# Optimization experiments

Measured on AMD Instinct MI355X. Metric: run time of the kernel, lower is better.

Reference implementation:

```python
import jax, jax.numpy as jnp
import numpy as np

B, N, DH, DG, HID, K_STEPS, CURV = 256, 2048, 128, 256, 256, 2, 1.0
SC = CURV ** 0.5
SCALE = 1.0 / (DH ** 0.5)
LN_EPS = 1e-5


def _artanh(x):
    return jnp.arctanh(jnp.clip(x, -1.0 + 1e-5, 1.0 - 1e-5))


def logmap0(x, sc=SC):
    n = jnp.maximum(jnp.linalg.norm(x, axis=-1, keepdims=True), 1e-7)
    return x * (_artanh(sc * n) / (sc * n))


def expmap0(v, sc=SC):
    n = jnp.maximum(jnp.linalg.norm(v, axis=-1, keepdims=True), 1e-7)
    return v * (jnp.tanh(sc * n) / (sc * n))


def setup_inputs() -> dict:
    key = jax.random.key(0)
    ks = jax.random.split(key, 16)

    def lin(k, out_d, in_d):
        return (jax.random.normal(k, (out_d, in_d), jnp.float32) * (in_d ** -0.5))

    demo_hyp = expmap0(0.1 * jax.random.normal(ks[0], (B, N, DH), jnp.float32))
    rho_g = jax.random.normal(ks[1], (B, DG), jnp.float32)
    return {
        "demo_hyp": demo_hyp,
        "rho_g": rho_g,
        "seed_g_w": lin(ks[2], DH, DG),
        "seed_g_b": jnp.zeros((DH,), jnp.float32),
        "seed_d_w": lin(ks[3], DH, DH),
        "pool_wq_w": lin(ks[4], DH, DH),
        "pool_wk_w": lin(ks[5], DH, DH),
        "pool_wv_w": lin(ks[6], DH, DH),
        "q_u_w": lin(ks[7], DH, DH),
        "q_g_w": lin(ks[8], DH, DG),
        "q_g_b": jnp.zeros((DH,), jnp.float32),
        "kv_w": lin(ks[9], DH, DH),
        "mlp_w1": lin(ks[10], HID, DH),
        "mlp_b1": jnp.zeros((HID,), jnp.float32),
        "mlp_w2": lin(ks[11], DH, HID),
        "mlp_b2": jnp.zeros((DH,), jnp.float32),
        "ln_g": jnp.ones((DH,), jnp.float32),
        "ln_b": jnp.zeros((DH,), jnp.float32),
    }


def reference(demo_hyp, rho_g, seed_g_w, seed_g_b, seed_d_w,
              pool_wq_w, pool_wk_w, pool_wv_w, q_u_w, q_g_w, q_g_b,
              kv_w, mlp_w1, mlp_b1, mlp_w2, mlp_b2, ln_g, ln_b):
    demo_tan = logmap0(demo_hyp)                       # (B,N,Dh)

    # seed: attention-pool demos with rho_g query
    q_seed = rho_g @ seed_g_w.T + seed_g_b             # (B,Dh)
    qk = q_seed @ pool_wq_w.T                          # (B,Dh)
    Kp = demo_tan @ pool_wk_w.T                        # (B,N,Dh)
    a = jax.nn.softmax(jnp.einsum('bd,bnd->bn', qk, Kp) * SCALE, axis=-1)
    Vp = demo_tan @ pool_wv_w.T
    pooled = jnp.einsum('bn,bnd->bd', a, Vp)           # (B,Dh)
    u = expmap0(q_seed + pooled @ seed_d_w.T)

    for _ in range(K_STEPS):
        u_tan = logmap0(u)
        mu = jnp.mean(u_tan, axis=-1, keepdims=True)
        var = jnp.var(u_tan, axis=-1, keepdims=True)
        u_tan = (u_tan - mu) * jax.lax.rsqrt(var + LN_EPS) * ln_g + ln_b
        q = u_tan @ q_u_w.T + rho_g @ q_g_w.T + q_g_b
        Kmat = demo_tan @ kv_w.T                       # keys == values
        att = jax.nn.softmax(jnp.einsum('bd,bnd->bn', q, Kmat) * SCALE, axis=-1)
        delta = jnp.einsum('bn,bnd->bd', att, Kmat)
        upd = jax.nn.gelu(delta @ mlp_w1.T + mlp_b1, approximate=False) @ mlp_w2.T + mlp_b2
        u = expmap0(u_tan + upd)
    return u
```

## Files before the change

kernel.cpp:

```cpp
#include <hip/hip_runtime.h>
#include <cstddef>
#include <cstdint>

#define B 256
#define N 2048
#define DH 128
#define DG 256
#define HID 256
#define WAVES 8
#define TPB (WAVES * 64)
#define RPI (WAVES * 8)
#define KIT (N / RPI)
#define SCALE 0.08838834764831845f
#define LN_EPS 1e-5f
#define TAN_NORM_MAX 6.2f


__device__ __forceinline__ float artanh_clip(float a) {
  a = fminf(a, 1.0f - 1e-5f);
  return 0.5f * __logf((1.0f + a) / (1.0f - a));
}

__device__ __forceinline__ float logmap_scale(float n2) {
  float nc = fmaxf(sqrtf(n2), 1e-7f);
  return artanh_clip(nc) / nc;
}

__device__ __forceinline__ float row16_sum(float x) {
  x += __int_as_float(__builtin_amdgcn_update_dpp(0, __float_as_int(x), 0x128, 0xF, 0xF, true));
  x += __int_as_float(__builtin_amdgcn_update_dpp(0, __float_as_int(x), 0x124, 0xF, 0xF, true));
  x += __int_as_float(__builtin_amdgcn_update_dpp(0, __float_as_int(x), 0x122, 0xF, 0xF, true));
  x += __int_as_float(__builtin_amdgcn_update_dpp(0, __float_as_int(x), 0x121, 0xF, 0xF, true));
  return x;
}

__device__ __forceinline__ float wave_allsum(float v) {
#pragma unroll
  for (int m = 1; m < 64; m <<= 1) v += __shfl_xor(v, m);
  return v;
}

__device__ __forceinline__ float dot128(const float* __restrict__ wrow,
                                        const float* __restrict__ x) {
  const float4* a = (const float4*)wrow;
  const float4* v = (const float4*)x;
  float s = 0.f;
#pragma unroll
  for (int j = 0; j < 32; ++j) {
    float4 u = a[j], b = v[j];
    s += u.x * b.x + u.y * b.y + u.z * b.z + u.w * b.w;
  }
  return s;
}

__device__ __forceinline__ float dot256(const float* __restrict__ wrow,
                                        const float* __restrict__ x) {
  const float4* a = (const float4*)wrow;
  const float4* v = (const float4*)x;
  float s = 0.f;
#pragma unroll
  for (int j = 0; j < 64; ++j) {
    float4 u = a[j], b = v[j];
    s += u.x * b.x + u.y * b.y + u.z * b.z + u.w * b.w;
  }
  return s;
}


__global__ __launch_bounds__(TPB, 2) void fused_refiner(
    const float* __restrict__ demo, const float* __restrict__ rho,
    const float* __restrict__ seed_g_w, const float* __restrict__ seed_g_b,
    const float* __restrict__ seed_d_w, const float* __restrict__ pool_wq_w,
    const float* __restrict__ pool_wk_w, const float* __restrict__ pool_wv_w,
    const float* __restrict__ q_u_w, const float* __restrict__ q_g_w,
    const float* __restrict__ q_g_b, const float* __restrict__ kv_w,
    const float* __restrict__ mlp_w1, const float* __restrict__ mlp_b1,
    const float* __restrict__ mlp_w2, const float* __restrict__ mlp_b2,
    const float* __restrict__ ln_g, const float* __restrict__ ln_b,
    float* __restrict__ out) {
  const int b = blockIdx.x;
  const int tid = threadIdx.x;
  const int w = tid >> 6;
  const int lane = tid & 63;
  const int g = lane >> 4;
  const int il = lane & 15;

  __shared__ __align__(16) float s_rho[DG];
  __shared__ __align__(16) float s_x[DH];
  __shared__ __align__(16) float s_y[DH];
  __shared__ __align__(16) float s_h[HID];
  __shared__ __align__(16) float s_ut[DH];
  __shared__ __align__(16) float s_qseed[DH];
  __shared__ __align__(16) float s_qvec[DH];
  __shared__ __align__(16) float s_fold[WAVES][DH];
  __shared__ float s_l[WAVES];
  __shared__ float s_red[WAVES];
  __shared__ float s_Mb;

  auto bsumAll = [&](float v) -> float {
    v = wave_allsum(v);
    if (lane == 0) s_red[w] = v;
    __syncthreads();
    float r = s_red[0] + s_red[1] + s_red[2] + s_red[3] +
              s_red[4] + s_red[5] + s_red[6] + s_red[7];
    __syncthreads();
    return r;
  };

  auto ln_query = [&](float v) {
    float n2 = bsumAll(tid < DH ? v * v : 0.f);
    float u = 0.f, ut = 0.f;
    if (tid < DH) {
      float nc = fmaxf(sqrtf(n2), 1e-7f);
      u = v * (tanhf(nc) / nc);
    }
    float nu2 = bsumAll(tid < DH ? u * u : 0.f);
    if (tid < DH) {
      float nuc = fmaxf(sqrtf(nu2), 1e-7f);
      ut = u * (artanh_clip(nuc) / nuc);
    }
    float mu = bsumAll(tid < DH ? ut : 0.f) * (1.0f / DH);
    float d = ut - mu;
    float var = bsumAll(tid < DH ? d * d : 0.f) * (1.0f / DH);
    if (tid < DH) {
      float y = d * rsqrtf(var + LN_EPS) * ln_g[tid] + ln_b[tid];
      s_ut[tid] = y;
      s_x[tid] = y;
    }
    __syncthreads();
    if (tid < DH) {
      s_y[tid] = q_g_b[tid] + dot128(q_u_w + (size_t)tid * DH, s_x) +
                 dot256(q_g_w + (size_t)tid * DG, s_rho);
    }
    __syncthreads();
    float qp = 0.f;
    if (tid < DH) {
#pragma unroll 8
      for (int i = 0; i < DH; ++i) qp += kv_w[i * DH + tid] * s_y[i];
      s_qvec[tid] = qp;
    }
    float qn2 = bsumAll(tid < DH ? qp * qp : 0.f);
    if (tid == 0) s_Mb = SCALE * TAN_NORM_MAX * sqrtf(qn2);
    __syncthreads();
  };

  if (tid < DG) s_rho[tid] = rho[(size_t)b * DG + tid];
  __syncthreads();
  if (tid < DH) {
    float qs = seed_g_b[tid] + dot256(seed_g_w + (size_t)tid * DG, s_rho);
    s_qseed[tid] = qs;
    s_x[tid] = qs;
  }
  __syncthreads();
  if (tid < DH) s_y[tid] = dot128(pool_wq_w + (size_t)tid * DH, s_x);
  __syncthreads();
  float qp0 = 0.f;
  if (tid < DH) {
#pragma unroll 8
    for (int i = 0; i < DH; ++i) qp0 += pool_wk_w[i * DH + tid] * s_y[i];
    s_qvec[tid] = qp0;
  }
  float qn2 = bsumAll(tid < DH ? qp0 * qp0 : 0.f);
  if (tid == 0) s_Mb = SCALE * TAN_NORM_MAX * sqrtf(qn2);
  __syncthreads();

  const float* demo_b = demo + (size_t)b * N * DH;

  for (int pass = 0; pass < 3; ++pass) {
    const float4 qv0 = *(const float4*)&s_qvec[il * 4];
    const float4 qv1 = *(const float4*)&s_qvec[64 + il * 4];
    const float Mb = s_Mb;
    const float* p = demo_b + (size_t)(w * 8 + g) * DH + il * 4;

    float lsum = 0.f;
    float4 accL = make_float4(0.f, 0.f, 0.f, 0.f);
    float4 accH = make_float4(0.f, 0.f, 0.f, 0.f);

    float4 xa1 = *(const float4*)(p);
    float4 xa2 = *(const float4*)(p + 64);
    float4 xb1 = *(const float4*)(p + 4 * DH);
    float4 xb2 = *(const float4*)(p + 4 * DH + 64);

    for (int k = 0; k < KIT; ++k) {
      float4 ca1 = xa1, ca2 = xa2, cb1 = xb1, cb2 = xb2;
      if (k + 1 < KIT) {
        const float* pn = p + (size_t)(k + 1) * RPI * DH;
        xa1 = *(const float4*)(pn);
        xa2 = *(const float4*)(pn + 64);
        xb1 = *(const float4*)(pn + 4 * DH);
        xb2 = *(const float4*)(pn + 4 * DH + 64);
      }
      {
        float dd = qv0.x * ca1.x + qv0.y * ca1.y + qv0.z * ca1.z + qv0.w * ca1.w +
                   qv1.x * ca2.x + qv1.y * ca2.y + qv1.z * ca2.z + qv1.w * ca2.w;
        float n2 = ca1.x * ca1.x + ca1.y * ca1.y + ca1.z * ca1.z + ca1.w * ca1.w +
                   ca2.x * ca2.x + ca2.y * ca2.y + ca2.z * ca2.z + ca2.w * ca2.w;
        dd = row16_sum(dd);
        n2 = row16_sum(n2);
        float tsv = logmap_scale(n2);
        float pw = __expf(dd * tsv * SCALE - Mb);
        lsum += pw;
        float c = pw * tsv;
        accL.x += c * ca1.x; accL.y += c * ca1.y; accL.z += c * ca1.z; accL.w += c * ca1.w;
        accH.x += c * ca2.x; accH.y += c * ca2.y; accH.z += c * ca2.z; accH.w += c * ca2.w;
      }
      {
        float dd = qv0.x * cb1.x + qv0.y * cb1.y + qv0.z * cb1.z + qv0.w * cb1.w +
                   qv1.x * cb2.x + qv1.y * cb2.y + qv1.z * cb2.z + qv1.w * cb2.w;
        float n2 = cb1.x * cb1.x + cb1.y * cb1.y + cb1.z * cb1.z + cb1.w * cb1.w +
                   cb2.x * cb2.x + cb2.y * cb2.y + cb2.z * cb2.z + cb2.w * cb2.w;
        dd = row16_sum(dd);
        n2 = row16_sum(n2);
        float tsv = logmap_scale(n2);
        float pw = __expf(dd * tsv * SCALE - Mb);
        lsum += pw;
        float c = pw * tsv;
        accL.x += c * cb1.x; accL.y += c * cb1.y; accL.z += c * cb1.z; accL.w += c * cb1.w;
        accH.x += c * cb2.x; accH.y += c * cb2.y; accH.z += c * cb2.z; accH.w += c * cb2.w;
      }
    }

    accL.x += __shfl_xor(accL.x, 16); accL.x += __shfl_xor(accL.x, 32);
    accL.y += __shfl_xor(accL.y, 16); accL.y += __shfl_xor(accL.y, 32);
    accL.z += __shfl_xor(accL.z, 16); accL.z += __shfl_xor(accL.z, 32);
    accL.w += __shfl_xor(accL.w, 16); accL.w += __shfl_xor(accL.w, 32);
    accH.x += __shfl_xor(accH.x, 16); accH.x += __shfl_xor(accH.x, 32);
    accH.y += __shfl_xor(accH.y, 16); accH.y += __shfl_xor(accH.y, 32);
    accH.z += __shfl_xor(accH.z, 16); accH.z += __shfl_xor(accH.z, 32);
    accH.w += __shfl_xor(accH.w, 16); accH.w += __shfl_xor(accH.w, 32);
    lsum += __shfl_xor(lsum, 16); lsum += __shfl_xor(lsum, 32);
    if (g == 0) {
      *(float4*)&s_fold[w][il * 4] = accL;
      *(float4*)&s_fold[w][64 + il * 4] = accH;
      if (il == 0) s_l[w] = lsum;
    }
    __syncthreads();

    if (tid < DH) {
      float a = 0.f;
#pragma unroll
      for (int j = 0; j < WAVES; ++j) a += s_fold[j][tid];
      float L = s_l[0] + s_l[1] + s_l[2] + s_l[3] +
                s_l[4] + s_l[5] + s_l[6] + s_l[7];
      s_x[tid] = a / L;
    }
    __syncthreads();

    if (pass == 0) {
      if (tid < DH) s_y[tid] = dot128(pool_wv_w + (size_t)tid * DH, s_x);
      __syncthreads();
      float v = 0.f;
      if (tid < DH) v = s_qseed[tid] + dot128(seed_d_w + (size_t)tid * DH, s_y);
      ln_query(v);
    } else {
      if (tid < DH) s_y[tid] = dot128(kv_w + (size_t)tid * DH, s_x);
      __syncthreads();
      if (tid < HID) {
        float h = mlp_b1[tid] + dot128(mlp_w1 + (size_t)tid * DH, s_y);
        s_h[tid] = 0.5f * h * (1.0f + erff(h * 0.70710678118654752f));
      }
      __syncthreads();
      float v = 0.f;
      if (tid < DH)
        v = s_ut[tid] + mlp_b2[tid] + dot256(mlp_w2 + (size_t)tid * HID, s_h);
      if (pass == 2) {
        float n2 = bsumAll(tid < DH ? v * v : 0.f);
        if (tid < DH) {
          float nc = fmaxf(sqrtf(n2), 1e-7f);
          out[(size_t)b * DH + tid] = v * (tanhf(nc) / nc);
        }
      } else {
        ln_query(v);
      }
    }
  }
}


extern "C" void kernel_launch(void* const* d_in, const int* in_sizes, int n_in,
                              void* d_out, int out_size, void* d_ws, size_t ws_size,
                              hipStream_t stream) {
  const float* demo      = (const float*)d_in[0];
  const float* rho       = (const float*)d_in[1];
  const float* seed_g_w  = (const float*)d_in[2];
  const float* seed_g_b  = (const float*)d_in[3];
  const float* seed_d_w  = (const float*)d_in[4];
  const float* pool_wq_w = (const float*)d_in[5];
  const float* pool_wk_w = (const float*)d_in[6];
  const float* pool_wv_w = (const float*)d_in[7];
  const float* q_u_w     = (const float*)d_in[8];
  const float* q_g_w     = (const float*)d_in[9];
  const float* q_g_b     = (const float*)d_in[10];
  const float* kv_w      = (const float*)d_in[11];
  const float* mlp_w1    = (const float*)d_in[12];
  const float* mlp_b1    = (const float*)d_in[13];
  const float* mlp_w2    = (const float*)d_in[14];
  const float* mlp_b2    = (const float*)d_in[15];
  const float* ln_g      = (const float*)d_in[16];
  const float* ln_b      = (const float*)d_in[17];
  float* out = (float*)d_out;
  (void)d_ws; (void)ws_size; (void)in_sizes; (void)n_in; (void)out_size;

  fused_refiner<<<B, TPB, 0, stream>>>(demo, rho, seed_g_w, seed_g_b, seed_d_w,
                                       pool_wq_w, pool_wk_w, pool_wv_w, q_u_w,
                                       q_g_w, q_g_b, kv_w, mlp_w1, mlp_b1,
                                       mlp_w2, mlp_b2, ln_g, ln_b, out);
}
```

Measured before the change: 516.8 us.

## Cache log-mapped demos in fp16 workspace and split passes into three kernels

The first pass computes the log-mapped demo rows once, writes them as fp16 into the workspace, and the two refinement passes read that half-size cache instead of re-reading fp32 demos and recomputing norms and artanh. This roughly halves demo traffic for two of the three passes and removes the per-row logmap math there. The single fused kernel is split into three launches with 16 waves per block, with per-batch state passed through global memory. In exchange it adds a 128 MiB fp16 write, launch overhead, and fp16 rounding error in the attention keys and values.

```diff
diff --git a/kernel.cpp b/kernel.cpp
--- a/kernel.cpp
+++ b/kernel.cpp
@@ -1,4 +1,5 @@
 #include <hip/hip_runtime.h>
+#include <hip/hip_fp16.h>
 #include <cstddef>
 #include <cstdint>
 
@@ -7,7 +8,7 @@
 #define DH 128
 #define DG 256
 #define HID 256
-#define WAVES 8
+#define WAVES 16
 #define TPB (WAVES * 64)
 #define RPI (WAVES * 8)
 #define KIT (N / RPI)
@@ -67,212 +68,328 @@
 }
 
 
-__global__ __launch_bounds__(TPB, 2) void fused_refiner(
+struct __align__(16) Smem {
+  float rho[DG];
+  float x[DH];
+  float y[DH];
+  float h[HID];
+  float ut[DH];
+  float qseed[DH];
+  float qvec[DH];
+  float fold[WAVES][DH];
+  float l[WAVES];
+  float red[WAVES];
+  float Mb;
+};
+
+__device__ __forceinline__ float bsumAll(Smem& sm, float v, int w, int lane) {
+  v = wave_allsum(v);
+  if (lane == 0) sm.red[w] = v;
+  __syncthreads();
+  float r = 0.f;
+#pragma unroll
+  for (int j = 0; j < WAVES; ++j) r += sm.red[j];
+  __syncthreads();
+  return r;
+}
+
+__device__ __forceinline__ void ln_query(Smem& sm, float v, int tid, int w, int lane,
+    const float* __restrict__ q_u_w, const float* __restrict__ q_g_w,
+    const float* __restrict__ q_g_b, const float* __restrict__ kv_w,
+    const float* __restrict__ ln_g, const float* __restrict__ ln_b) {
+  float n2 = bsumAll(sm, tid < DH ? v * v : 0.f, w, lane);
+  float u = 0.f, ut = 0.f;
+  if (tid < DH) {
+    float nc = fmaxf(sqrtf(n2), 1e-7f);
+    u = v * (tanhf(nc) / nc);
+  }
+  float nu2 = bsumAll(sm, tid < DH ? u * u : 0.f, w, lane);
+  if (tid < DH) {
+    float nuc = fmaxf(sqrtf(nu2), 1e-7f);
+    ut = u * (artanh_clip(nuc) / nuc);
+  }
+  float mu = bsumAll(sm, tid < DH ? ut : 0.f, w, lane) * (1.0f / DH);
+  float d = ut - mu;
+  float var = bsumAll(sm, tid < DH ? d * d : 0.f, w, lane) * (1.0f / DH);
+  if (tid < DH) {
+    float y = d * rsqrtf(var + LN_EPS) * ln_g[tid] + ln_b[tid];
+    sm.ut[tid] = y;
+    sm.x[tid] = y;
+  }
+  __syncthreads();
+  if (tid < DH) {
+    sm.y[tid] = q_g_b[tid] + dot128(q_u_w + (size_t)tid * DH, sm.x) +
+                dot256(q_g_w + (size_t)tid * DG, sm.rho);
+  }
+  __syncthreads();
+  float qp = 0.f;
+  if (tid < DH) {
+#pragma unroll 8
+    for (int i = 0; i < DH; ++i) qp += kv_w[i * DH + tid] * sm.y[i];
+    sm.qvec[tid] = qp;
+  }
+  float qn2 = bsumAll(sm, tid < DH ? qp * qp : 0.f, w, lane);
+  if (tid == 0) sm.Mb = SCALE * TAN_NORM_MAX * sqrtf(qn2);
+  __syncthreads();
+}
+
+__device__ __forceinline__ void fold_combine(Smem& sm, float4 accL, float4 accH,
+                                             float lsum, int w, int g, int il, int tid) {
+  accL.x += __shfl_xor(accL.x, 16); accL.x += __shfl_xor(accL.x, 32);
+  accL.y += __shfl_xor(accL.y, 16); accL.y += __shfl_xor(accL.y, 32);
+  accL.z += __shfl_xor(accL.z, 16); accL.z += __shfl_xor(accL.z, 32);
+  accL.w += __shfl_xor(accL.w, 16); accL.w += __shfl_xor(accL.w, 32);
+  accH.x += __shfl_xor(accH.x, 16); accH.x += __shfl_xor(accH.x, 32);
+  accH.y += __shfl_xor(accH.y, 16); accH.y += __shfl_xor(accH.y, 32);
+  accH.z += __shfl_xor(accH.z, 16); accH.z += __shfl_xor(accH.z, 32);
+  accH.w += __shfl_xor(accH.w, 16); accH.w += __shfl_xor(accH.w, 32);
+  lsum += __shfl_xor(lsum, 16); lsum += __shfl_xor(lsum, 32);
+  if (g == 0) {
+    *(float4*)&sm.fold[w][il * 4] = accL;
+    *(float4*)&sm.fold[w][64 + il * 4] = accH;
+    if (il == 0) sm.l[w] = lsum;
+  }
+  __syncthreads();
+  if (tid < DH) {
+    float a = 0.f, L = 0.f;
+#pragma unroll
+    for (int j = 0; j < WAVES; ++j) { a += sm.fold[j][tid]; L += sm.l[j]; }
+    sm.x[tid] = a / L;
+  }
+  __syncthreads();
+}
+
+__device__ __forceinline__ void proc_fp32(const float4 c1, const float4 c2,
+    const float4 qv0, const float4 qv1, const float Mb,
+    __half* __restrict__ yw,
+    float& lsum, float4& accL, float4& accH) {
+  float dd = qv0.x * c1.x + qv0.y * c1.y + qv0.z * c1.z + qv0.w * c1.w +
+             qv1.x * c2.x + qv1.y * c2.y + qv1.z * c2.z + qv1.w * c2.w;
+  float n2 = c1.x * c1.x + c1.y * c1.y + c1.z * c1.z + c1.w * c1.w +
+             c2.x * c2.x + c2.y * c2.y + c2.z * c2.z + c2.w * c2.w;
+  dd = row16_sum(dd);
+  n2 = row16_sum(n2);
+  float tsv = logmap_scale(n2);
+  float4 y1 = make_float4(tsv * c1.x, tsv * c1.y, tsv * c1.z, tsv * c1.w);
+  float4 y2 = make_float4(tsv * c2.x, tsv * c2.y, tsv * c2.z, tsv * c2.w);
+  __half2 h01 = __float22half2_rn(make_float2(y1.x, y1.y));
+  __half2 h23 = __float22half2_rn(make_float2(y1.z, y1.w));
+  __half2 h45 = __float22half2_rn(make_float2(y2.x, y2.y));
+  __half2 h67 = __float22half2_rn(make_float2(y2.z, y2.w));
+  uint4 pk;
+  pk.x = *(const unsigned*)&h01; pk.y = *(const unsigned*)&h23;
+  pk.z = *(const unsigned*)&h45; pk.w = *(const unsigned*)&h67;
+  *(uint4*)yw = pk;
+  float pw = __expf(dd * tsv * SCALE - Mb);
+  lsum += pw;
+  accL.x += pw * y1.x; accL.y += pw * y1.y; accL.z += pw * y1.z; accL.w += pw * y1.w;
+  accH.x += pw * y2.x; accH.y += pw * y2.y; accH.z += pw * y2.z; accH.w += pw * y2.w;
+}
+
+__device__ __forceinline__ void proc_fp16(const uint4 pk,
+    const float4 qv0, const float4 qv1, const float Mb,
+    float& lsum, float4& accL, float4& accH) {
+  float2 f0 = __half22float2(*(const __half2*)&pk.x);
+  float2 f1 = __half22float2(*(const __half2*)&pk.y);
+  float2 f2 = __half22float2(*(const __half2*)&pk.z);
+  float2 f3 = __half22float2(*(const __half2*)&pk.w);
+  float dd = qv0.x * f0.x + qv0.y * f0.y + qv0.z * f1.x + qv0.w * f1.y +
+             qv1.x * f2.x + qv1.y * f2.y + qv1.z * f3.x + qv1.w * f3.y;
+  dd = row16_sum(dd);
+  float pw = __expf(dd * SCALE - Mb);
+  lsum += pw;
+  accL.x += pw * f0.x; accL.y += pw * f0.y; accL.z += pw * f1.x; accL.w += pw * f1.y;
+  accH.x += pw * f2.x; accH.y += pw * f2.y; accH.z += pw * f3.x; accH.w += pw * f3.y;
+}
+
+
+__global__ __launch_bounds__(TPB) void refine_a(
     const float* __restrict__ demo, const float* __restrict__ rho,
     const float* __restrict__ seed_g_w, const float* __restrict__ seed_g_b,
     const float* __restrict__ seed_d_w, const float* __restrict__ pool_wq_w,
     const float* __restrict__ pool_wk_w, const float* __restrict__ pool_wv_w,
     const float* __restrict__ q_u_w, const float* __restrict__ q_g_w,
     const float* __restrict__ q_g_b, const float* __restrict__ kv_w,
+    const float* __restrict__ ln_g, const float* __restrict__ ln_b,
+    __half* __restrict__ ycache, float* __restrict__ g_ut,
+    float* __restrict__ g_qvec, float* __restrict__ g_mb) {
+  __shared__ Smem sm;
+  const int b = blockIdx.x, tid = threadIdx.x;
+  const int w = tid >> 6, lane = tid & 63;
+  const int g = lane >> 4, il = lane & 15;
+
+  if (tid < DG) sm.rho[tid] = rho[(size_t)b * DG + tid];
+  __syncthreads();
+  if (tid < DH) {
+    float qs = seed_g_b[tid] + dot256(seed_g_w + (size_t)tid * DG, sm.rho);
+    sm.qseed[tid] = qs;
+    sm.x[tid] = qs;
+  }
+  __syncthreads();
+  if (tid < DH) sm.y[tid] = dot128(pool_wq_w + (size_t)tid * DH, sm.x);
+  __syncthreads();
+  float qp0 = 0.f;
+  if (tid < DH) {
+#pragma unroll 8
+    for (int i = 0; i < DH; ++i) qp0 += pool_wk_w[i * DH + tid] * sm.y[i];
+    sm.qvec[tid] = qp0;
+  }
+  float qn2 = bsumAll(sm, tid < DH ? qp0 * qp0 : 0.f, w, lane);
+  if (tid == 0) sm.Mb = SCALE * TAN_NORM_MAX * sqrtf(qn2);
+  __syncthreads();
+
+  const float* p = demo + (size_t)b * N * DH + (size_t)(w * 8 + g) * DH + il * 4;
+  __half* yw = ycache + (size_t)b * N * DH + (size_t)(w * 8 + g) * DH + (size_t)il * 8;
+  const float4 qv0 = *(const float4*)&sm.qvec[il * 4];
+  const float4 qv1 = *(const float4*)&sm.qvec[64 + il * 4];
+  const float Mb = sm.Mb;
+
+  float lsum = 0.f;
+  float4 accL = make_float4(0.f, 0.f, 0.f, 0.f);
+  float4 accH = make_float4(0.f, 0.f, 0.f, 0.f);
+
+#define LD4(s1, s2, s3, s4, kk)                                   \
+  do {                                                            \
+    const float* pn_ = p + (size_t)(kk) * RPI * DH;               \
+    s1 = *(const float4*)(pn_);                                   \
+    s2 = *(const float4*)(pn_ + 64);                              \
+    s3 = *(const float4*)(pn_ + 4 * DH);                          \
+    s4 = *(const float4*)(pn_ + 4 * DH + 64);                     \
+  } while (0)
+
+  float4 a1A, a2A, b1A, b2A, a1B, a2B, b1B, b2B;
+  LD4(a1A, a2A, b1A, b2A, 0);
+  LD4(a1B, a2B, b1B, b2B, 1);
+
+  for (int k = 0; k < KIT; k += 2) {
+    {
+      float4 c1 = a1A, c2 = a2A, d1 = b1A, d2 = b2A;
+      if (k + 2 < KIT) LD4(a1A, a2A, b1A, b2A, k + 2);
+      proc_fp32(c1, c2, qv0, qv1, Mb, yw + (size_t)k * RPI * DH, lsum, accL, accH);
+      proc_fp32(d1, d2, qv0, qv1, Mb, yw + (size_t)k * RPI * DH + 4 * DH, lsum, accL, accH);
+    }
+    {
+      float4 c1 = a1B, c2 = a2B, d1 = b1B, d2 = b2B;
+      if (k + 3 < KIT) LD4(a1B, a2B, b1B, b2B, k + 3);
+      proc_fp32(c1, c2, qv0, qv1, Mb, yw + (size_t)(k + 1) * RPI * DH, lsum, accL, accH);
+      proc_fp32(d1, d2, qv0, qv1, Mb, yw + (size_t)(k + 1) * RPI * DH + 4 * DH, lsum, accL, accH);
+    }
+  }
+#undef LD4
+
+  fold_combine(sm, accL, accH, lsum, w, g, il, tid);
+
+  if (tid < DH) sm.y[tid] = dot128(pool_wv_w + (size_t)tid * DH, sm.x);
+  __syncthreads();
+  float v = 0.f;
+  if (tid < DH) v = sm.qseed[tid] + dot128(seed_d_w + (size_t)tid * DH, sm.y);
+  ln_query(sm, v, tid, w, lane, q_u_w, q_g_w, q_g_b, kv_w, ln_g, ln_b);
+  if (tid < DH) {
+    g_ut[(size_t)b * DH + tid] = sm.ut[tid];
+    g_qvec[(size_t)b * DH + tid] = sm.qvec[tid];
+  }
+  if (tid == 0) g_mb[b] = sm.Mb;
+}
+
+
+template <int FINAL>
+__global__ __launch_bounds__(TPB) void refine_bc(
+    const float* __restrict__ rho, const float* __restrict__ kv_w,
     const float* __restrict__ mlp_w1, const float* __restrict__ mlp_b1,
     const float* __restrict__ mlp_w2, const float* __restrict__ mlp_b2,
-    const float* __restrict__ ln_g, const float* __restrict__ ln_b,
-    float* __restrict__ out) {
-  const int b = blockIdx.x;
-  const int tid = threadIdx.x;
-  const int w = tid >> 6;
-  const int lane = tid & 63;
-  const int g = lane >> 4;
-  const int il = lane & 15;
-
-  __shared__ __align__(16) float s_rho[DG];
-  __shared__ __align__(16) float s_x[DH];
-  __shared__ __align__(16) float s_y[DH];
-  __shared__ __align__(16) float s_h[HID];
-  __shared__ __align__(16) float s_ut[DH];
-  __shared__ __align__(16) float s_qseed[DH];
-  __shared__ __align__(16) float s_qvec[DH];
-  __shared__ __align__(16) float s_fold[WAVES][DH];
-  __shared__ float s_l[WAVES];
-  __shared__ float s_red[WAVES];
-  __shared__ float s_Mb;
-
-  auto bsumAll = [&](float v) -> float {
-    v = wave_allsum(v);
-    if (lane == 0) s_red[w] = v;
-    __syncthreads();
-    float r = s_red[0] + s_red[1] + s_red[2] + s_red[3] +
-              s_red[4] + s_red[5] + s_red[6] + s_red[7];
-    __syncthreads();
-    return r;
-  };
-
-  auto ln_query = [&](float v) {
-    float n2 = bsumAll(tid < DH ? v * v : 0.f);
-    float u = 0.f, ut = 0.f;
+    const float* __restrict__ q_u_w, const float* __restrict__ q_g_w,
+    const float* __restrict__ q_g_b, const float* __restrict__ ln_g,
+    const float* __restrict__ ln_b, const __half* __restrict__ ycache,
+    float* __restrict__ g_ut, float* __restrict__ g_qvec,
+    float* __restrict__ g_mb, float* __restrict__ out) {
+  __shared__ Smem sm;
+  const int b = blockIdx.x, tid = threadIdx.x;
+  const int w = tid >> 6, lane = tid & 63;
+  const int g = lane >> 4, il = lane & 15;
+
+  if (tid < DG) sm.rho[tid] = rho[(size_t)b * DG + tid];
+  if (tid < DH) {
+    sm.qvec[tid] = g_qvec[(size_t)b * DH + tid];
+    sm.ut[tid] = g_ut[(size_t)b * DH + tid];
+  }
+  if (tid == 0) sm.Mb = g_mb[b];
+  __syncthreads();
+
+  const __half* yr = ycache + (size_t)b * N * DH + (size_t)(w * 8 + g) * DH + (size_t)il * 8;
+  const float4 qv0 = *(const float4*)&sm.qvec[il * 4];
+  const float4 qv1 = *(const float4*)&sm.qvec[64 + il * 4];
+  const float Mb = sm.Mb;
+
+  float lsum = 0.f;
+  float4 accL = make_float4(0.f, 0.f, 0.f, 0.f);
+  float4 accH = make_float4(0.f, 0.f, 0.f, 0.f);
+
+#define LDY(sa, sb, kk)                                           \
+  do {                                                            \
+    const __half* pn_ = yr + (size_t)(kk) * RPI * DH;             \
+    sa = *(const uint4*)(pn_);                                    \
+    sb = *(const uint4*)(pn_ + 4 * DH);                           \
+  } while (0)
+
+  uint4 y0a, y0b, y1a, y1b, y2a, y2b, y3a, y3b;
+  LDY(y0a, y0b, 0);
+  LDY(y1a, y1b, 1);
+  LDY(y2a, y2b, 2);
+  LDY(y3a, y3b, 3);
+
+  for (int k = 0; k < KIT; k += 4) {
+    {
+      uint4 pa = y0a, pb = y0b;
+      if (k + 4 < KIT) LDY(y0a, y0b, k + 4);
+      proc_fp16(pa, qv0, qv1, Mb, lsum, accL, accH);
+      proc_fp16(pb, qv0, qv1, Mb, lsum, accL, accH);
+    }
+    {
+      uint4 pa = y1a, pb = y1b;
+      if (k + 5 < KIT) LDY(y1a, y1b, k + 5);
+      proc_fp16(pa, qv0, qv1, Mb, lsum, accL, accH);
+      proc_fp16(pb, qv0, qv1, Mb, lsum, accL, accH);
+    }
+    {
+      uint4 pa = y2a, pb = y2b;
+      if (k + 6 < KIT) LDY(y2a, y2b, k + 6);
+      proc_fp16(pa, qv0, qv1, Mb, lsum, accL, accH);
+      proc_fp16(pb, qv0, qv1, Mb, lsum, accL, accH);
+    }
+    {
+      uint4 pa = y3a, pb = y3b;
+      if (k + 7 < KIT) LDY(y3a, y3b, k + 7);
+      proc_fp16(pa, qv0, qv1, Mb, lsum, accL, accH);
+      proc_fp16(pb, qv0, qv1, Mb, lsum, accL, accH);
+    }
+  }
+#undef LDY
+
+  fold_combine(sm, accL, accH, lsum, w, g, il, tid);
+
+  if (tid < DH) sm.y[tid] = dot128(kv_w + (size_t)tid * DH, sm.x);
+  __syncthreads();
+  if (tid < HID) {
+    float hh = mlp_b1[tid] + dot128(mlp_w1 + (size_t)tid * DH, sm.y);
+    sm.h[tid] = 0.5f * hh * (1.0f + erff(hh * 0.70710678118654752f));
+  }
+  __syncthreads();
+  float v = 0.f;
+  if (tid < DH)
+    v = sm.ut[tid] + mlp_b2[tid] + dot256(mlp_w2 + (size_t)tid * HID, sm.h);
+  if (FINAL) {
+    float n2 = bsumAll(sm, tid < DH ? v * v : 0.f, w, lane);
     if (tid < DH) {
       float nc = fmaxf(sqrtf(n2), 1e-7f);
-      u = v * (tanhf(nc) / nc);
-    }
-    float nu2 = bsumAll(tid < DH ? u * u : 0.f);
+      out[(size_t)b * DH + tid] = v * (tanhf(nc) / nc);
+    }
+  } else {
+    ln_query(sm, v, tid, w, lane, q_u_w, q_g_w, q_g_b, kv_w, ln_g, ln_b);
     if (tid < DH) {
-      float nuc = fmaxf(sqrtf(nu2), 1e-7f);
-      ut = u * (artanh_clip(nuc) / nuc);
-    }
-    float mu = bsumAll(tid < DH ? ut : 0.f) * (1.0f / DH);
-    float d = ut - mu;
-    float var = bsumAll(tid < DH ? d * d : 0.f) * (1.0f / DH);
-    if (tid < DH) {
-      float y = d * rsqrtf(var + LN_EPS) * ln_g[tid] + ln_b[tid];
-      s_ut[tid] = y;
-      s_x[tid] = y;
-    }
-    __syncthreads();
-    if (tid < DH) {
-      s_y[tid] = q_g_b[tid] + dot128(q_u_w + (size_t)tid * DH, s_x) +
-                 dot256(q_g_w + (size_t)tid * DG, s_rho);
-    }
-    __syncthreads();
-    float qp = 0.f;
-    if (tid < DH) {
-#pragma unroll 8
-      for (int i = 0; i < DH; ++i) qp += kv_w[i * DH + tid] * s_y[i];
-      s_qvec[tid] = qp;
-    }
-    float qn2 = bsumAll(tid < DH ? qp * qp : 0.f);
-    if (tid == 0) s_Mb = SCALE * TAN_NORM_MAX * sqrtf(qn2);
-    __syncthreads();
-  };
-
-  if (tid < DG) s_rho[tid] = rho[(size_t)b * DG + tid];
-  __syncthreads();
-  if (tid < DH) {
-    float qs = seed_g_b[tid] + dot256(seed_g_w + (size_t)tid * DG, s_rho);
-    s_qseed[tid] = qs;
-    s_x[tid] = qs;
-  }
-  __syncthreads();
-  if (tid < DH) s_y[tid] = dot128(pool_wq_w + (size_t)tid * DH, s_x);
-  __syncthreads();
-  float qp0 = 0.f;
-  if (tid < DH) {
-#pragma unroll 8
-    for (int i = 0; i < DH; ++i) qp0 += pool_wk_w[i * DH + tid] * s_y[i];
-    s_qvec[tid] = qp0;
-  }
-  float qn2 = bsumAll(tid < DH ? qp0 * qp0 : 0.f);
-  if (tid == 0) s_Mb = SCALE * TAN_NORM_MAX * sqrtf(qn2);
-  __syncthreads();
-
-  const float* demo_b = demo + (size_t)b * N * DH;
-
-  for (int pass = 0; pass < 3; ++pass) {
-    const float4 qv0 = *(const float4*)&s_qvec[il * 4];
-    const float4 qv1 = *(const float4*)&s_qvec[64 + il * 4];
-    const float Mb = s_Mb;
-    const float* p = demo_b + (size_t)(w * 8 + g) * DH + il * 4;
-
-    float lsum = 0.f;
-    float4 accL = make_float4(0.f, 0.f, 0.f, 0.f);
-    float4 accH = make_float4(0.f, 0.f, 0.f, 0.f);
-
-    float4 xa1 = *(const float4*)(p);
-    float4 xa2 = *(const float4*)(p + 64);
-    float4 xb1 = *(const float4*)(p + 4 * DH);
-    float4 xb2 = *(const float4*)(p + 4 * DH + 64);
-
-    for (int k = 0; k < KIT; ++k) {
-      float4 ca1 = xa1, ca2 = xa2, cb1 = xb1, cb2 = xb2;
-      if (k + 1 < KIT) {
-        const float* pn = p + (size_t)(k + 1) * RPI * DH;
-        xa1 = *(const float4*)(pn);
-        xa2 = *(const float4*)(pn + 64);
-        xb1 = *(const float4*)(pn + 4 * DH);
-        xb2 = *(const float4*)(pn + 4 * DH + 64);
-      }
-      {
-        float dd = qv0.x * ca1.x + qv0.y * ca1.y + qv0.z * ca1.z + qv0.w * ca1.w +
-                   qv1.x * ca2.x + qv1.y * ca2.y + qv1.z * ca2.z + qv1.w * ca2.w;
-        float n2 = ca1.x * ca1.x + ca1.y * ca1.y + ca1.z * ca1.z + ca1.w * ca1.w +
-                   ca2.x * ca2.x + ca2.y * ca2.y + ca2.z * ca2.z + ca2.w * ca2.w;
-        dd = row16_sum(dd);
-        n2 = row16_sum(n2);
-        float tsv = logmap_scale(n2);
-        float pw = __expf(dd * tsv * SCALE - Mb);
-        lsum += pw;
-        float c = pw * tsv;
-        accL.x += c * ca1.x; accL.y += c * ca1.y; accL.z += c * ca1.z; accL.w += c * ca1.w;
-        accH.x += c * ca2.x; accH.y += c * ca2.y; accH.z += c * ca2.z; accH.w += c * ca2.w;
-      }
-      {
-        float dd = qv0.x * cb1.x + qv0.y * cb1.y + qv0.z * cb1.z + qv0.w * cb1.w +
-                   qv1.x * cb2.x + qv1.y * cb2.y + qv1.z * cb2.z + qv1.w * cb2.w;
-        float n2 = cb1.x * cb1.x + cb1.y * cb1.y + cb1.z * cb1.z + cb1.w * cb1.w +
-                   cb2.x * cb2.x + cb2.y * cb2.y + cb2.z * cb2.z + cb2.w * cb2.w;
-        dd = row16_sum(dd);
-        n2 = row16_sum(n2);
-        float tsv = logmap_scale(n2);
-        float pw = __expf(dd * tsv * SCALE - Mb);
-        lsum += pw;
-        float c = pw * tsv;
-        accL.x += c * cb1.x; accL.y += c * cb1.y; accL.z += c * cb1.z; accL.w += c * cb1.w;
-        accH.x += c * cb2.x; accH.y += c * cb2.y; accH.z += c * cb2.z; accH.w += c * cb2.w;
-      }
-    }
-
-    accL.x += __shfl_xor(accL.x, 16); accL.x += __shfl_xor(accL.x, 32);
-    accL.y += __shfl_xor(accL.y, 16); accL.y += __shfl_xor(accL.y, 32);
-    accL.z += __shfl_xor(accL.z, 16); accL.z += __shfl_xor(accL.z, 32);
-    accL.w += __shfl_xor(accL.w, 16); accL.w += __shfl_xor(accL.w, 32);
-    accH.x += __shfl_xor(accH.x, 16); accH.x += __shfl_xor(accH.x, 32);
-    accH.y += __shfl_xor(accH.y, 16); accH.y += __shfl_xor(accH.y, 32);
-    accH.z += __shfl_xor(accH.z, 16); accH.z += __shfl_xor(accH.z, 32);
-    accH.w += __shfl_xor(accH.w, 16); accH.w += __shfl_xor(accH.w, 32);
-    lsum += __shfl_xor(lsum, 16); lsum += __shfl_xor(lsum, 32);
-    if (g == 0) {
-      *(float4*)&s_fold[w][il * 4] = accL;
-      *(float4*)&s_fold[w][64 + il * 4] = accH;
-      if (il == 0) s_l[w] = lsum;
-    }
-    __syncthreads();
-
-    if (tid < DH) {
-      float a = 0.f;
-#pragma unroll
-      for (int j = 0; j < WAVES; ++j) a += s_fold[j][tid];
-      float L = s_l[0] + s_l[1] + s_l[2] + s_l[3] +
-                s_l[4] + s_l[5] + s_l[6] + s_l[7];
-      s_x[tid] = a / L;
-    }
-    __syncthreads();
-
-    if (pass == 0) {
-      if (tid < DH) s_y[tid] = dot128(pool_wv_w + (size_t)tid * DH, s_x);
-      __syncthreads();
-      float v = 0.f;
-      if (tid < DH) v = s_qseed[tid] + dot128(seed_d_w + (size_t)tid * DH, s_y);
-      ln_query(v);
-    } else {
-      if (tid < DH) s_y[tid] = dot128(kv_w + (size_t)tid * DH, s_x);
-      __syncthreads();
-      if (tid < HID) {
-        float h = mlp_b1[tid] + dot128(mlp_w1 + (size_t)tid * DH, s_y);
-        s_h[tid] = 0.5f * h * (1.0f + erff(h * 0.70710678118654752f));
-      }
-      __syncthreads();
-      float v = 0.f;
-      if (tid < DH)
-        v = s_ut[tid] + mlp_b2[tid] + dot256(mlp_w2 + (size_t)tid * HID, s_h);
-      if (pass == 2) {
-        float n2 = bsumAll(tid < DH ? v * v : 0.f);
-        if (tid < DH) {
-          float nc = fmaxf(sqrtf(n2), 1e-7f);
-          out[(size_t)b * DH + tid] = v * (tanhf(nc) / nc);
-        }
-      } else {
-        ln_query(v);
-      }
-    }
+      g_ut[(size_t)b * DH + tid] = sm.ut[tid];
+      g_qvec[(size_t)b * DH + tid] = sm.qvec[tid];
+    }
+    if (tid == 0) g_mb[b] = sm.Mb;
   }
 }
 
@@ -299,10 +416,22 @@
   const float* ln_g      = (const float*)d_in[16];
   const float* ln_b      = (const float*)d_in[17];
   float* out = (float*)d_out;
-  (void)d_ws; (void)ws_size; (void)in_sizes; (void)n_in; (void)out_size;
-
-  fused_refiner<<<B, TPB, 0, stream>>>(demo, rho, seed_g_w, seed_g_b, seed_d_w,
-                                       pool_wq_w, pool_wk_w, pool_wv_w, q_u_w,
-                                       q_g_w, q_g_b, kv_w, mlp_w1, mlp_b1,
-                                       mlp_w2, mlp_b2, ln_g, ln_b, out);
-}
+
+  __half* ycache = (__half*)d_ws;
+  float* fw = (float*)(ycache + (size_t)B * N * DH);
+  float* g_ut   = fw;
+  float* g_qvec = fw + (size_t)B * DH;
+  float* g_mb   = fw + (size_t)2 * B * DH;
+  (void)ws_size; (void)in_sizes; (void)n_in; (void)out_size;
+
+  refine_a<<<B, TPB, 0, stream>>>(demo, rho, seed_g_w, seed_g_b, seed_d_w,
+                                  pool_wq_w, pool_wk_w, pool_wv_w, q_u_w, q_g_w,
+                                  q_g_b, kv_w, ln_g, ln_b, ycache, g_ut, g_qvec,
+                                  g_mb);
+  refine_bc<0><<<B, TPB, 0, stream>>>(rho, kv_w, mlp_w1, mlp_b1, mlp_w2, mlp_b2,
+                                      q_u_w, q_g_w, q_g_b, ln_g, ln_b, ycache,
+                                      g_ut, g_qvec, g_mb, out);
+  refine_bc<1><<<B, TPB, 0, stream>>>(rho, kv_w, mlp_w1, mlp_b1, mlp_w2, mlp_b2,
+                                      q_u_w, q_g_w, q_g_b, ln_g, ln_b, ycache,
+                                      g_ut, g_qvec, g_mb, out);
+}
```

Measured after the change: 524.2 us. About the same (+1.4%).
